# Performance work log

Hardware: AMD Instinct MI355X
Metric: run time of the kernel (lower is better)

## Reference

```python
import jax, jax.numpy as jnp
import numpy as np

N_NODES = 8192
ADJ_LEN = 4096  # first half of codebook = adjective nodes, rest = noun nodes
E_DIM = 256
TOPK = 4
BETA = 0.25


def setup_inputs() -> dict:
    key = jax.random.key(0)
    ks = jax.random.split(key, 6)
    z = jax.random.normal(ks[0], (64, 2 * E_DIM, 16, 16), dtype=jnp.float32)
    node_x = jax.random.normal(ks[1], (N_NODES, 1024), dtype=jnp.float32)
    edge_index = jax.random.randint(ks[2], (2, 131072), 0, N_NODES, dtype=jnp.int32)
    W1 = jax.random.normal(ks[3], (1024, E_DIM), dtype=jnp.float32) * 0.02
    b1 = jnp.zeros((E_DIM,), dtype=jnp.float32)
    W2 = jax.random.normal(ks[4], (E_DIM, E_DIM), dtype=jnp.float32) * 0.02
    b2 = jnp.zeros((E_DIM,), dtype=jnp.float32)
    return {"z": z, "node_x": node_x, "edge_index": edge_index,
            "W1": W1, "b1": b1, "W2": W2, "b2": b2}


def gcn_conv(x, edge_index, W, b):
    # GCNConv: symmetric-normalized adjacency with self-loops, then linear.
    n = x.shape[0]
    loop = jnp.arange(n, dtype=edge_index.dtype)
    src = jnp.concatenate([edge_index[0], loop])
    dst = jnp.concatenate([edge_index[1], loop])
    xw = x @ W  # [n, out]
    deg = jax.ops.segment_sum(jnp.ones_like(dst, dtype=xw.dtype), dst, num_segments=n)
    dinv = jax.lax.rsqrt(jnp.maximum(deg, 1e-12))
    norm = dinv[src] * dinv[dst]  # [E+n]
    out = jax.ops.segment_sum(norm[:, None] * xw[src], dst, num_segments=n)
    return out + b


def pairwise_sqdist(zf, emb):
    # ||z||^2 + ||e||^2 - 2 z.e  -> [M, K]
    return (jnp.sum(zf * zf, axis=1, keepdims=True)
            + jnp.sum(emb * emb, axis=1)
            - 2.0 * zf @ emb.T)


def reference(z, node_x, edge_index, W1, b1, W2, b2):
    sg = jax.lax.stop_gradient
    # GCN over codebook graph (eval mode: dropout is identity)
    h = jax.nn.relu(gcn_conv(node_x, edge_index, W1, b1))
    tew = gcn_conv(h, edge_index, W2, b2)  # [N_NODES, E_DIM]

    b, c2, H, W = z.shape
    # ---- adjective branch: top-k gather + mean ----
    z_adj = jnp.transpose(z[:, :E_DIM], (0, 2, 3, 1))  # b h w c
    zf = z_adj.reshape(-1, E_DIM)  # [M, e_dim]
    emb_a = tew[:ADJ_LEN]
    d = pairwise_sqdist(zf, emb_a)
    _, idx1 = jax.lax.top_k(-d, TOPK)  # [M, topk] smallest distances
    z_adj_q = emb_a[idx1].mean(axis=1).reshape(z_adj.shape)

    quan_loss = jnp.mean((sg(z_adj_q) - z_adj) ** 2)
    commit_loss = BETA * jnp.mean((z_adj_q - sg(z_adj)) ** 2)
    loss = quan_loss + commit_loss
    z_adj_q = z_adj + sg(z_adj_q - z_adj)  # straight-through
    z_adj_q = jnp.transpose(z_adj_q, (0, 3, 1, 2))
    ind1 = idx1.reshape(b, H * W * TOPK)  # sane_index_shape, c=256

    # ---- noun branch: argmin ----
    z_noun = jnp.transpose(z[:, E_DIM:], (0, 2, 3, 1))
    zf = z_noun.reshape(-1, E_DIM)
    emb_n = tew[ADJ_LEN:]
    d = pairwise_sqdist(zf, emb_n)
    idx2 = jnp.argmin(d, axis=1)  # [M]
    z_noun_q = emb_n[idx2].reshape(z_noun.shape)

    q2 = jnp.mean((sg(z_noun_q) - z_noun) ** 2)
    c2_ = BETA * jnp.mean((z_noun_q - sg(z_noun)) ** 2)
    loss = loss + q2 + c2_
    commit_loss = commit_loss + c2_
    quan_loss = quan_loss + q2
    z_noun_q = z_noun + sg(z_noun_q - z_noun)
    z_noun_q = jnp.transpose(z_noun_q, (0, 3, 1, 2))
    ind2 = idx2.reshape(b, H * W)

    z_q = jnp.concatenate([z_adj_q, z_noun_q], axis=1)
    indices = jnp.concatenate([ind1, ind2], axis=1)
    return z_q, loss, commit_loss, quan_loss, indices
```

## Files before the change

kernel.cpp:

```cpp
#include <hip/hip_runtime.h>

#define N_NODES 8192
#define N_EDGES 131072
#define E_DIM 256
#define NE_HALF 4096
#define LOSS_OFF 8388608
#define IDX_OFF 8388611
#define KC_PANEL 384

#define WS_DINV 0
#define WS_EN2 8192
#define WS_LOSS 16384
#define WS_CNT 17408
#define WS_ROWSTART 25600
#define WS_FILL 34816
#define WS_COL 43008
#define WS_XW 174080
#define WS_H  2271232
#define WS_TEW 4368384
#define WS_QN2 6465536

__global__ void count_kernel(const int* __restrict__ dst, int* __restrict__ cnt) {
    int e = blockIdx.x * blockDim.x + threadIdx.x;
    if (e < N_EDGES) atomicAdd(&cnt[dst[e]], 1);
}

__global__ __launch_bounds__(1024) void scan_kernel(const int* __restrict__ cnt,
                                                    int* __restrict__ rowstart,
                                                    float* __restrict__ dinv) {
    __shared__ int part[1024];
    int t = threadIdx.x;
    int c[8], pre[8];
    int run = 0;
#pragma unroll
    for (int i = 0; i < 8; ++i) {
        c[i] = cnt[t * 8 + i];
        pre[i] = run;
        run += c[i];
    }
    part[t] = run;
    __syncthreads();
    for (int d = 1; d < 1024; d <<= 1) {
        int add = (t >= d) ? part[t - d] : 0;
        __syncthreads();
        part[t] += add;
        __syncthreads();
    }
    int off = (t == 0) ? 0 : part[t - 1];
#pragma unroll
    for (int i = 0; i < 8; ++i) {
        rowstart[t * 8 + i] = off + pre[i];
        dinv[t * 8 + i] = 1.0f / sqrtf((float)(c[i] + 1));
    }
    if (t == 1023) rowstart[8192] = part[1023];
}

__global__ void scatter_kernel(const int* __restrict__ dst,
                               const int* __restrict__ rowstart, int* __restrict__ fill,
                               int* __restrict__ col) {
    int e = blockIdx.x * blockDim.x + threadIdx.x;
    if (e < N_EDGES) {
        int d = dst[e];
        int pos = atomicAdd(&fill[d], 1);
        col[rowstart[d] + pos] = e;
    }
}

__global__ __launch_bounds__(256) void sort_kernel(const int* __restrict__ src,
                                                   const int* __restrict__ rowstart,
                                                   int* __restrict__ col) {
    int i = blockIdx.x * blockDim.x + threadIdx.x;
    if (i >= N_NODES) return;
    int s0 = rowstart[i], s1 = rowstart[i + 1];
    for (int a = s0 + 1; a < s1; ++a) {
        int v = col[a];
        int b = a - 1;
        while (b >= s0 && col[b] > v) { col[b + 1] = col[b]; --b; }
        col[b + 1] = v;
    }
    for (int a = s0; a < s1; ++a) col[a] = src[col[a]];
}

__global__ __launch_bounds__(256) void gemm_kernel(const float* __restrict__ X,
                                                   const float* __restrict__ W,
                                                   float* __restrict__ Y, int K) {
    __shared__ float aT[16][68];
    __shared__ float bT[16][68];
    const int t = threadIdx.x;
    const int bm = blockIdx.x * 64;
    const int bn = blockIdx.y * 64;
    float cacc[4][4] = {};
    const int tm = t >> 4, tn = t & 15;
    const int lm = t >> 2, lk = (t & 3) * 4;
    const int bk = t >> 4, bn4 = (t & 15) * 4;
    int kp = 0;
    bool first = true;
    while (kp < K) {
        int rem = K - kp;
        int pl;
        if (rem >= 2 * KC_PANEL) pl = KC_PANEL;
        else if (rem > KC_PANEL) pl = (rem / 2 + 15) & ~15;
        else pl = rem;
        const int kend = kp + pl;
        float pacc[4][4] = {};
        for (int k0 = kp; k0 < kend; k0 += 16) {
            __syncthreads();
            float4 av = *(const float4*)&X[(size_t)(bm + lm) * K + k0 + lk];
            aT[lk + 0][lm] = av.x; aT[lk + 1][lm] = av.y;
            aT[lk + 2][lm] = av.z; aT[lk + 3][lm] = av.w;
            *(float4*)&bT[bk][bn4] = *(const float4*)&W[(size_t)(k0 + bk) * E_DIM + bn + bn4];
            __syncthreads();
#pragma unroll
            for (int k = 0; k < 16; ++k) {
                float4 a = *(const float4*)&aT[k][tm * 4];
                float4 b = *(const float4*)&bT[k][tn * 4];
                float qa[4] = {a.x, a.y, a.z, a.w};
                float ea[4] = {b.x, b.y, b.z, b.w};
#pragma unroll
                for (int i = 0; i < 4; ++i)
#pragma unroll
                    for (int j = 0; j < 4; ++j) pacc[i][j] = fmaf(qa[i], ea[j], pacc[i][j]);
            }
        }
        if (first) {
#pragma unroll
            for (int i = 0; i < 4; ++i)
#pragma unroll
                for (int j = 0; j < 4; ++j) cacc[i][j] = pacc[i][j];
        } else {
#pragma unroll
            for (int i = 0; i < 4; ++i)
#pragma unroll
                for (int j = 0; j < 4; ++j) cacc[i][j] = __fadd_rn(cacc[i][j], pacc[i][j]);
        }
        first = false;
        kp = kend;
    }
#pragma unroll
    for (int i = 0; i < 4; ++i) {
        float4 v = make_float4(cacc[i][0], cacc[i][1], cacc[i][2], cacc[i][3]);
        *(float4*)&Y[(size_t)(bm + tm * 4 + i) * E_DIM + bn + tn * 4] = v;
    }
}

__global__ __launch_bounds__(256) void agg_kernel(const float* __restrict__ xw,
                                                  const int* __restrict__ rowstart,
                                                  const int* __restrict__ col,
                                                  const float* __restrict__ dinv,
                                                  const float* __restrict__ bias,
                                                  float* __restrict__ out, int do_relu) {
    int i = blockIdx.x;
    int c = threadIdx.x;
    float di = dinv[i];
    float acc = 0.0f;
    int s0 = rowstart[i], s1 = rowstart[i + 1];
    for (int j = s0; j < s1; ++j) {
        int s = col[j];
        float nrm = __fmul_rn(dinv[s], di);
        acc = __fadd_rn(acc, __fmul_rn(nrm, xw[(size_t)s * E_DIM + c]));
    }
    acc = __fadd_rn(acc, __fmul_rn(__fmul_rn(di, di), xw[(size_t)i * E_DIM + c]));
    acc = __fadd_rn(acc, bias[c]);
    if (do_relu) acc = fmaxf(acc, 0.0f);
    out[(size_t)i * E_DIM + c] = acc;
}

__global__ __launch_bounds__(256) void enorm_kernel(const float* __restrict__ e,
                                                    float* __restrict__ out) {
    int t = threadIdx.x;
    int row = blockIdx.x * 16 + (t >> 4);
    int l = t & 15;
    int blk = l >> 3, j = l & 7;
    const float* p = e + (size_t)row * 256 + blk * 128 + j;
    float v = p[0];
    float acc = __fmul_rn(v, v);
#pragma unroll
    for (int i = 1; i < 16; ++i) {
        float w = p[i * 8];
        acc = __fadd_rn(acc, __fmul_rn(w, w));
    }
    acc = __fadd_rn(acc, __shfl_xor(acc, 1, 64));
    acc = __fadd_rn(acc, __shfl_xor(acc, 2, 64));
    acc = __fadd_rn(acc, __shfl_xor(acc, 4, 64));
    acc = __fadd_rn(acc, __shfl_xor(acc, 8, 64));
    if (l == 0) out[row] = acc;
}

__global__ __launch_bounds__(256) void qnorm_kernel(const float* __restrict__ z,
                                                    float* __restrict__ out) {
    int t = threadIdx.x;
    int row = blockIdx.x * 16 + (t >> 4);
    int half = row >> 14, r = row & 16383;
    int b = r >> 8, pp = r & 255;
    int l = t & 15;
    int blk = l >> 3, j = l & 7;
    const float* p = z + (size_t)b * 131072 + (size_t)half * 65536 + pp +
                     (size_t)(blk * 128 + j) * 256;
    float v = p[0];
    float acc = __fmul_rn(v, v);
#pragma unroll
    for (int i = 1; i < 16; ++i) {
        float w = p[(size_t)i * 8 * 256];
        acc = __fadd_rn(acc, __fmul_rn(w, w));
    }
    acc = __fadd_rn(acc, __shfl_xor(acc, 1, 64));
    acc = __fadd_rn(acc, __shfl_xor(acc, 2, 64));
    acc = __fadd_rn(acc, __shfl_xor(acc, 4, 64));
    acc = __fadd_rn(acc, __shfl_xor(acc, 8, 64));
    if (l == 0) out[row] = acc;
}

template <int TK>
__global__ __launch_bounds__(256) void quant_kernel(const float* __restrict__ z,
                                                    const float* __restrict__ emb,
                                                    const float* __restrict__ en2,
                                                    const float* __restrict__ qn2,
                                                    float* __restrict__ out,
                                                    float* __restrict__ lossAcc, int coff) {
    __shared__ float qT[E_DIM][36];
    __shared__ float eT[32][132];
    __shared__ float sEn2[128];
    __shared__ int sIdx[32][TK];
    __shared__ float red[256];

    const int t = threadIdx.x;
    const int r0 = blockIdx.x * 32;
    const int b = r0 >> 8;
    const int p0 = r0 & 255;

    {
        const int q = t & 31;
        const int kk = t >> 5;
        const float* zb = z + (size_t)b * 131072 + (size_t)coff * 256 + (p0 + q);
#pragma unroll
        for (int i = 0; i < 32; ++i) {
            int k = kk + 8 * i;
            qT[k][q] = zb[(size_t)k * 256];
        }
    }

    const int tq = t >> 5;
    const int te = t & 31;
    const int q0 = tq * 4;
    const int e0 = te * 4;
    const int sk = (t & 7) * 4;
    const int se = t >> 3;

    float aq[4];
#pragma unroll
    for (int i = 0; i < 4; ++i) aq[i] = qn2[r0 + q0 + i];

    float bsr[4][TK];
    int bir[4][TK];
#pragma unroll
    for (int i = 0; i < 4; ++i)
#pragma unroll
        for (int j = 0; j < TK; ++j) { bsr[i][j] = 3.4e38f; bir[i][j] = 0; }

    for (int et = 0; et < NE_HALF / 128; ++et) {
        const int ebase = et * 128;
        float acc[4][4] = {};
        for (int kc = 0; kc < 8; ++kc) {
            __syncthreads();
#pragma unroll
            for (int i = 0; i < 4; ++i) {
                int e = se + 32 * i;
                float4 v = *(const float4*)&emb[(size_t)(ebase + e) * E_DIM + kc * 32 + sk];
                eT[sk + 0][e] = v.x; eT[sk + 1][e] = v.y;
                eT[sk + 2][e] = v.z; eT[sk + 3][e] = v.w;
            }
            if (kc == 0 && t < 128) sEn2[t] = en2[ebase + t];
            __syncthreads();
#pragma unroll 8
            for (int k = 0; k < 32; ++k) {
                float4 qv = *(const float4*)&qT[kc * 32 + k][q0];
                float4 ev = *(const float4*)&eT[k][e0];
                float qa[4] = {qv.x, qv.y, qv.z, qv.w};
                float ea[4] = {ev.x, ev.y, ev.z, ev.w};
#pragma unroll
                for (int i = 0; i < 4; ++i)
#pragma unroll
                    for (int j = 0; j < 4; ++j) acc[i][j] = fmaf(qa[i], ea[j], acc[i][j]);
            }
        }
#pragma unroll
        for (int j = 0; j < 4; ++j) {
            float e2 = sEn2[e0 + j];
            int gi = ebase + e0 + j;
#pragma unroll
            for (int i = 0; i < 4; ++i) {
                float t1 = __fadd_rn(aq[i], e2);
                float s = __fsub_rn(t1, __fmul_rn(2.0f, acc[i][j]));
                if (s < bsr[i][TK - 1]) {
                    bsr[i][TK - 1] = s; bir[i][TK - 1] = gi;
#pragma unroll
                    for (int m = TK - 1; m > 0; --m) {
                        if (bsr[i][m] < bsr[i][m - 1]) {
                            float tf = bsr[i][m]; bsr[i][m] = bsr[i][m - 1]; bsr[i][m - 1] = tf;
                            int ti2 = bir[i][m]; bir[i][m] = bir[i][m - 1]; bir[i][m - 1] = ti2;
                        }
                    }
                }
            }
        }
    }

#pragma unroll
    for (int m = 1; m < 32; m <<= 1) {
#pragma unroll
        for (int i = 0; i < 4; ++i) {
            float ms[TK], os[TK], ns[TK];
            int mi[TK], oi[TK], ni[TK];
#pragma unroll
            for (int j = 0; j < TK; ++j) {
                ms[j] = bsr[i][j]; mi[j] = bir[i][j];
                os[j] = __shfl_xor(bsr[i][j], m, 64);
                oi[j] = __shfl_xor(bir[i][j], m, 64);
            }
#pragma unroll
            for (int x = 0; x < TK; ++x) {
                bool ta = (ms[0] < os[0]) || (ms[0] == os[0] && mi[0] < oi[0]);
                ns[x] = ta ? ms[0] : os[0];
                ni[x] = ta ? mi[0] : oi[0];
#pragma unroll
                for (int y = 0; y < TK - 1; ++y) {
                    ms[y] = ta ? ms[y + 1] : ms[y];
                    mi[y] = ta ? mi[y + 1] : mi[y];
                    os[y] = ta ? os[y] : os[y + 1];
                    oi[y] = ta ? oi[y] : oi[y + 1];
                }
            }
#pragma unroll
            for (int j = 0; j < TK; ++j) { bsr[i][j] = ns[j]; bir[i][j] = ni[j]; }
        }
    }

    if (te == 0) {
#pragma unroll
        for (int i = 0; i < 4; ++i) {
            int q = q0 + i;
            int r = r0 + q, bb = r >> 8, pp = r & 255;
#pragma unroll
            for (int j = 0; j < TK; ++j) sIdx[q][j] = bir[i][j];
            if (TK == 4) {
#pragma unroll
                for (int j = 0; j < TK; ++j)
                    out[IDX_OFF + (size_t)bb * 1280 + pp * 4 + j] = (float)bir[i][j];
            } else {
                out[IDX_OFF + (size_t)bb * 1280 + 1024 + pp] = (float)bir[i][0];
            }
        }
    }
    __syncthreads();

    float lsum = 0.0f;
    {
        const int q = t & 31;
        const int r = r0 + q, bb = r >> 8, pp = r & 255;
        float* ob = out + (size_t)bb * 131072 + (size_t)coff * 256 + pp;
        int id[TK];
#pragma unroll
        for (int j = 0; j < TK; ++j) id[j] = sIdx[q][j];
        const float inv = 1.0f / (float)TK;
        for (int i = 0; i < 32; ++i) {
            int c = (t >> 5) + 8 * i;
            float v = 0.0f;
#pragma unroll
            for (int j = 0; j < TK; ++j) v = __fadd_rn(v, emb[(size_t)id[j] * E_DIM + c]);
            v *= inv;
            float dd = v - qT[c][q];
            lsum += dd * dd;
            ob[(size_t)c * 256] = v;
        }
    }
    red[t] = lsum;
    __syncthreads();
    for (int s2 = 128; s2 > 0; s2 >>= 1) {
        if (t < s2) red[t] += red[t + s2];
        __syncthreads();
    }
    if (t == 0) atomicAdd(lossAcc, red[0]);
}

__global__ void final_kernel(const float* __restrict__ lossAcc, float* __restrict__ out) {
    if (threadIdx.x == 0 && blockIdx.x == 0) {
        const float inv = 1.0f / 4194304.0f;
        float mseA = lossAcc[0] * inv;
        float mseN = lossAcc[1] * inv;
        float quan = mseA + mseN;
        float commit = 0.25f * mseA + 0.25f * mseN;
        out[LOSS_OFF + 0] = quan + commit;
        out[LOSS_OFF + 1] = commit;
        out[LOSS_OFF + 2] = quan;
    }
}

extern "C" void kernel_launch(void* const* d_in, const int* in_sizes, int n_in,
                              void* d_out, int out_size, void* d_ws, size_t ws_size,
                              hipStream_t stream) {
    const float* z = (const float*)d_in[0];
    const float* node_x = (const float*)d_in[1];
    const int* ei = (const int*)d_in[2];
    const float* W1 = (const float*)d_in[3];
    const float* b1 = (const float*)d_in[4];
    const float* W2 = (const float*)d_in[5];
    const float* b2 = (const float*)d_in[6];
    float* out = (float*)d_out;
    float* ws = (float*)d_ws;

    float* dinv = ws + WS_DINV;
    float* en2 = ws + WS_EN2;
    float* lossAcc = ws + WS_LOSS;
    int* cnt = (int*)(ws + WS_CNT);
    int* rowstart = (int*)(ws + WS_ROWSTART);
    int* fill = (int*)(ws + WS_FILL);
    int* col = (int*)(ws + WS_COL);
    float* xw = ws + WS_XW;
    float* h = ws + WS_H;
    float* tew = ws + WS_TEW;
    float* qn2 = ws + WS_QN2;

    const int* srcp = ei;
    const int* dstp = ei + N_EDGES;

    hipMemsetAsync(cnt, 0, N_NODES * sizeof(int), stream);
    hipMemsetAsync(fill, 0, N_NODES * sizeof(int), stream);
    hipMemsetAsync(lossAcc, 0, 2 * sizeof(float), stream);

    count_kernel<<<N_EDGES / 256, 256, 0, stream>>>(dstp, cnt);
    scan_kernel<<<1, 1024, 0, stream>>>(cnt, rowstart, dinv);
    scatter_kernel<<<N_EDGES / 256, 256, 0, stream>>>(dstp, rowstart, fill, col);
    sort_kernel<<<N_NODES / 256, 256, 0, stream>>>(srcp, rowstart, col);

    qnorm_kernel<<<2048, 256, 0, stream>>>(z, qn2);

    gemm_kernel<<<dim3(128, 4), 256, 0, stream>>>(node_x, W1, xw, 1024);
    agg_kernel<<<N_NODES, 256, 0, stream>>>(xw, rowstart, col, dinv, b1, h, 1);
    gemm_kernel<<<dim3(128, 4), 256, 0, stream>>>(h, W2, xw, 256);
    agg_kernel<<<N_NODES, 256, 0, stream>>>(xw, rowstart, col, dinv, b2, tew, 0);

    enorm_kernel<<<512, 256, 0, stream>>>(tew, en2);

    quant_kernel<4><<<512, 256, 0, stream>>>(z, tew, en2, qn2, out, lossAcc + 0, 0);
    quant_kernel<1><<<512, 256, 0, stream>>>(z, tew + (size_t)NE_HALF * E_DIM,
                                             en2 + NE_HALF, qn2 + 16384, out,
                                             lossAcc + 1, 256);
    final_kernel<<<1, 64, 0, stream>>>(lossAcc, out);
}
```

Measured before the change: 1.585 ms.

## Split codebook search across blocks with packed-key top-k and separate merge kernels

The distance/top-k search is split along the codebook dimension, so each block handles a slice of embeddings with a larger register tile (4 or 8 queries by 8 embeddings per thread), and partial top-k lists go to workspace. New merge kernels combine the partial lists, write indices, gather the quantized vectors and accumulate the losses. Distance and index are packed into one 64-bit key, which turns the comparisons and shuffles into single-word operations, and the shared-memory embedding tile uses an XOR swizzle to avoid bank conflicts. The cost is extra launches and a workspace round trip, plus higher register pressure from the bigger tiles. The packed key relies on the float bits ordering correctly as unsigned integers, which holds only for non-negative distances.

New measurement: 1.820 ms. 14.8% more time.

```diff
diff --git a/kernel.cpp b/kernel.cpp
--- a/kernel.cpp
+++ b/kernel.cpp
@@ -210,165 +210,276 @@
     if (l == 0) out[row] = acc;
 }
 
-template <int TK>
-__global__ __launch_bounds__(256) void quant_kernel(const float* __restrict__ z,
-                                                    const float* __restrict__ emb,
-                                                    const float* __restrict__ en2,
-                                                    const float* __restrict__ qn2,
-                                                    float* __restrict__ out,
-                                                    float* __restrict__ lossAcc, int coff) {
-    __shared__ float qT[E_DIM][36];
-    __shared__ float eT[32][132];
-    __shared__ float sEn2[128];
-    __shared__ int sIdx[32][TK];
+__device__ __forceinline__ unsigned long long shfl_xor_u64(unsigned long long v, int m) {
+    unsigned int lo = (unsigned int)v, hi = (unsigned int)(v >> 32);
+    lo = __shfl_xor(lo, m, 64);
+    hi = __shfl_xor(hi, m, 64);
+    return ((unsigned long long)hi << 32) | lo;
+}
+
+template <int TK, int QM>
+__device__ __forceinline__ void quant_body(const float* __restrict__ z,
+                                           const float* __restrict__ emb,
+                                           const float* __restrict__ en2,
+                                           const float* __restrict__ qn2,
+                                           unsigned long long* __restrict__ topWs,
+                                           int coff) {
+    constexpr int EP = QM / 2;
+    constexpr int QB = 8 * QM;
+    constexpr int EPB = NE_HALF / EP;
+    constexpr int NET = EPB / 256;
+    constexpr int QPAD = QB + 8;
+
+    __shared__ float eT[32][264];
+    __shared__ float qS[32][QPAD];
+    __shared__ float sEn2[256];
+
+    const int t = threadIdx.x;
+    const int qt = blockIdx.x / EP;
+    const int ep = blockIdx.x % EP;
+    const int r0 = qt * QB;
+    const int b = r0 >> 8;
+    const int p0 = r0 & 255;
+    const int e00 = ep * EPB;
+
+    const int tq = t >> 5, te = t & 31;
+    const int q0 = tq * QM;
+    const int e0 = te * 4;
+
+    const int sk = (t & 7) * 4;
+    const int se = t >> 3;
+    const int cb = se ^ (sk & 24);
+    const int kq = t >> 3, jq = (t & 7) * 4;
+
+    const float* zb = z + (size_t)b * 131072 + (size_t)coff * 256 + p0;
+
+    float aq[QM];
+#pragma unroll
+    for (int i = 0; i < QM; ++i) aq[i] = qn2[r0 + q0 + i];
+
+    unsigned long long bk[QM][TK];
+#pragma unroll
+    for (int i = 0; i < QM; ++i)
+#pragma unroll
+        for (int j = 0; j < TK; ++j) bk[i][j] = 0xFFFFFFFFFFFFFFFFull;
+
+    for (int et = 0; et < NET; ++et) {
+        const int ebase = e00 + et * 256;
+        float acc[QM][8] = {};
+        for (int kc = 0; kc < 8; ++kc) {
+            __syncthreads();
+#pragma unroll
+            for (int i = 0; i < 8; ++i) {
+                float4 v = *(const float4*)&emb[(size_t)(ebase + se + 32 * i) * 256 + kc * 32 + sk];
+                eT[sk + 0][cb + 32 * i] = v.x;
+                eT[sk + 1][cb + 32 * i] = v.y;
+                eT[sk + 2][cb + 32 * i] = v.z;
+                eT[sk + 3][cb + 32 * i] = v.w;
+            }
+            {
+                float4 v = *(const float4*)&zb[(size_t)(kc * 32 + kq) * 256 + jq];
+                *(float4*)&qS[kq][jq] = v;
+                if (QM == 8) {
+                    float4 w = *(const float4*)&zb[(size_t)(kc * 32 + kq) * 256 + jq + 32];
+                    *(float4*)&qS[kq][jq + 32] = w;
+                }
+            }
+            if (kc == 0) sEn2[t] = en2[ebase + t];
+            __syncthreads();
+#pragma unroll
+            for (int k = 0; k < 32; ++k) {
+                const int f = k & 24;
+                const int c1 = e0 ^ f;
+                float4 ea = *(const float4*)&eT[k][c1];
+                float4 eb = *(const float4*)&eT[k][128 + c1];
+                float ev[8] = {ea.x, ea.y, ea.z, ea.w, eb.x, eb.y, eb.z, eb.w};
+                float qv[QM];
+                {
+                    float4 qa = *(const float4*)&qS[k][q0];
+                    qv[0] = qa.x; qv[1] = qa.y; qv[2] = qa.z; qv[3] = qa.w;
+                    if (QM == 8) {
+                        float4 qb2 = *(const float4*)&qS[k][q0 + 4];
+                        qv[4] = qb2.x; qv[5] = qb2.y; qv[6] = qb2.z; qv[7] = qb2.w;
+                    }
+                }
+#pragma unroll
+                for (int i = 0; i < QM; ++i)
+#pragma unroll
+                    for (int j = 0; j < 8; ++j)
+                        acc[i][j] = fmaf(qv[i], ev[j], acc[i][j]);
+            }
+        }
+#pragma unroll
+        for (int j = 0; j < 8; ++j) {
+            const int le = (j < 4) ? (e0 + j) : (128 + e0 + j - 4);
+            float e2 = sEn2[le];
+            unsigned int gi = (unsigned int)(ebase + le);
+#pragma unroll
+            for (int i = 0; i < QM; ++i) {
+                float t1 = __fadd_rn(aq[i], e2);
+                float s = __fsub_rn(t1, __fmul_rn(2.0f, acc[i][j]));
+                unsigned long long key =
+                    ((unsigned long long)__float_as_uint(s) << 32) | gi;
+                if (key < bk[i][TK - 1]) {
+                    bk[i][TK - 1] = key;
+#pragma unroll
+                    for (int mm = TK - 1; mm > 0; --mm)
+                        if (bk[i][mm] < bk[i][mm - 1]) {
+                            unsigned long long tmp = bk[i][mm];
+                            bk[i][mm] = bk[i][mm - 1];
+                            bk[i][mm - 1] = tmp;
+                        }
+                }
+            }
+        }
+    }
+
+#pragma unroll
+    for (int mw = 1; mw < 32; mw <<= 1) {
+#pragma unroll
+        for (int i = 0; i < QM; ++i) {
+            unsigned long long ms[TK], os[TK], ns[TK];
+#pragma unroll
+            for (int j = 0; j < TK; ++j) {
+                ms[j] = bk[i][j];
+                os[j] = shfl_xor_u64(bk[i][j], mw);
+            }
+#pragma unroll
+            for (int x = 0; x < TK; ++x) {
+                bool ta = ms[0] < os[0];
+                ns[x] = ta ? ms[0] : os[0];
+#pragma unroll
+                for (int y = 0; y < TK - 1; ++y) {
+                    ms[y] = ta ? ms[y + 1] : ms[y];
+                    os[y] = ta ? os[y] : os[y + 1];
+                }
+            }
+#pragma unroll
+            for (int j = 0; j < TK; ++j) bk[i][j] = ns[j];
+        }
+    }
+
+    if (te == 0) {
+#pragma unroll
+        for (int i = 0; i < QM; ++i) {
+            unsigned long long* dst = topWs + ((size_t)(r0 + q0 + i) * EP + ep) * TK;
+#pragma unroll
+            for (int j = 0; j < TK; ++j) dst[j] = bk[i][j];
+        }
+    }
+}
+
+__global__ __launch_bounds__(256, 4) void quantA_kernel(const float* __restrict__ z,
+                                                        const float* __restrict__ emb,
+                                                        const float* __restrict__ en2,
+                                                        const float* __restrict__ qn2,
+                                                        unsigned long long* __restrict__ topWs) {
+    quant_body<4, 4>(z, emb, en2, qn2, topWs, 0);
+}
+
+__global__ __launch_bounds__(256, 3) void quantN_kernel(const float* __restrict__ z,
+                                                        const float* __restrict__ emb,
+                                                        const float* __restrict__ en2,
+                                                        const float* __restrict__ qn2,
+                                                        unsigned long long* __restrict__ topWs) {
+    quant_body<1, 8>(z, emb, en2, qn2, topWs, 256);
+}
+
+__global__ __launch_bounds__(256) void mergeA_kernel(const unsigned long long* __restrict__ topWs,
+                                                     const float* __restrict__ z,
+                                                     const float* __restrict__ emb,
+                                                     float* __restrict__ out,
+                                                     float* __restrict__ lossAcc) {
+    __shared__ int sIdx[32][4];
     __shared__ float red[256];
-
     const int t = threadIdx.x;
     const int r0 = blockIdx.x * 32;
-    const int b = r0 >> 8;
-    const int p0 = r0 & 255;
-
-    {
-        const int q = t & 31;
-        const int kk = t >> 5;
-        const float* zb = z + (size_t)b * 131072 + (size_t)coff * 256 + (p0 + q);
-#pragma unroll
-        for (int i = 0; i < 32; ++i) {
-            int k = kk + 8 * i;
-            qT[k][q] = zb[(size_t)k * 256];
-        }
-    }
-
-    const int tq = t >> 5;
-    const int te = t & 31;
-    const int q0 = tq * 4;
-    const int e0 = te * 4;
-    const int sk = (t & 7) * 4;
-    const int se = t >> 3;
-
-    float aq[4];
-#pragma unroll
-    for (int i = 0; i < 4; ++i) aq[i] = qn2[r0 + q0 + i];
-
-    float bsr[4][TK];
-    int bir[4][TK];
-#pragma unroll
-    for (int i = 0; i < 4; ++i)
-#pragma unroll
-        for (int j = 0; j < TK; ++j) { bsr[i][j] = 3.4e38f; bir[i][j] = 0; }
-
-    for (int et = 0; et < NE_HALF / 128; ++et) {
-        const int ebase = et * 128;
-        float acc[4][4] = {};
-        for (int kc = 0; kc < 8; ++kc) {
-            __syncthreads();
-#pragma unroll
-            for (int i = 0; i < 4; ++i) {
-                int e = se + 32 * i;
-                float4 v = *(const float4*)&emb[(size_t)(ebase + e) * E_DIM + kc * 32 + sk];
-                eT[sk + 0][e] = v.x; eT[sk + 1][e] = v.y;
-                eT[sk + 2][e] = v.z; eT[sk + 3][e] = v.w;
-            }
-            if (kc == 0 && t < 128) sEn2[t] = en2[ebase + t];
-            __syncthreads();
-#pragma unroll 8
-            for (int k = 0; k < 32; ++k) {
-                float4 qv = *(const float4*)&qT[kc * 32 + k][q0];
-                float4 ev = *(const float4*)&eT[k][e0];
-                float qa[4] = {qv.x, qv.y, qv.z, qv.w};
-                float ea[4] = {ev.x, ev.y, ev.z, ev.w};
-#pragma unroll
-                for (int i = 0; i < 4; ++i)
-#pragma unroll
-                    for (int j = 0; j < 4; ++j) acc[i][j] = fmaf(qa[i], ea[j], acc[i][j]);
-            }
-        }
+    const int b = r0 >> 8, p0 = r0 & 255;
+    if (t < 32) {
+        const unsigned long long* src = topWs + (size_t)(r0 + t) * 8;
+        unsigned long long ms[4], os[4], ns[4];
+#pragma unroll
+        for (int j = 0; j < 4; ++j) { ms[j] = src[j]; os[j] = src[4 + j]; }
+#pragma unroll
+        for (int x = 0; x < 4; ++x) {
+            bool ta = ms[0] < os[0];
+            ns[x] = ta ? ms[0] : os[0];
+#pragma unroll
+            for (int y = 0; y < 3; ++y) {
+                ms[y] = ta ? ms[y + 1] : ms[y];
+                os[y] = ta ? os[y] : os[y + 1];
+            }
+        }
+        int pp = p0 + t;
 #pragma unroll
         for (int j = 0; j < 4; ++j) {
-            float e2 = sEn2[e0 + j];
-            int gi = ebase + e0 + j;
-#pragma unroll
-            for (int i = 0; i < 4; ++i) {
-                float t1 = __fadd_rn(aq[i], e2);
-                float s = __fsub_rn(t1, __fmul_rn(2.0f, acc[i][j]));
-                if (s < bsr[i][TK - 1]) {
-                    bsr[i][TK - 1] = s; bir[i][TK - 1] = gi;
-#pragma unroll
-                    for (int m = TK - 1; m > 0; --m) {
-                        if (bsr[i][m] < bsr[i][m - 1]) {
-                            float tf = bsr[i][m]; bsr[i][m] = bsr[i][m - 1]; bsr[i][m - 1] = tf;
-                            int ti2 = bir[i][m]; bir[i][m] = bir[i][m - 1]; bir[i][m - 1] = ti2;
-                        }
-                    }
-                }
-            }
-        }
-    }
-
-#pragma unroll
-    for (int m = 1; m < 32; m <<= 1) {
-#pragma unroll
-        for (int i = 0; i < 4; ++i) {
-            float ms[TK], os[TK], ns[TK];
-            int mi[TK], oi[TK], ni[TK];
-#pragma unroll
-            for (int j = 0; j < TK; ++j) {
-                ms[j] = bsr[i][j]; mi[j] = bir[i][j];
-                os[j] = __shfl_xor(bsr[i][j], m, 64);
-                oi[j] = __shfl_xor(bir[i][j], m, 64);
-            }
-#pragma unroll
-            for (int x = 0; x < TK; ++x) {
-                bool ta = (ms[0] < os[0]) || (ms[0] == os[0] && mi[0] < oi[0]);
-                ns[x] = ta ? ms[0] : os[0];
-                ni[x] = ta ? mi[0] : oi[0];
-#pragma unroll
-                for (int y = 0; y < TK - 1; ++y) {
-                    ms[y] = ta ? ms[y + 1] : ms[y];
-                    mi[y] = ta ? mi[y + 1] : mi[y];
-                    os[y] = ta ? os[y] : os[y + 1];
-                    oi[y] = ta ? oi[y] : oi[y + 1];
-                }
-            }
-#pragma unroll
-            for (int j = 0; j < TK; ++j) { bsr[i][j] = ns[j]; bir[i][j] = ni[j]; }
-        }
-    }
-
-    if (te == 0) {
-#pragma unroll
-        for (int i = 0; i < 4; ++i) {
-            int q = q0 + i;
-            int r = r0 + q, bb = r >> 8, pp = r & 255;
-#pragma unroll
-            for (int j = 0; j < TK; ++j) sIdx[q][j] = bir[i][j];
-            if (TK == 4) {
-#pragma unroll
-                for (int j = 0; j < TK; ++j)
-                    out[IDX_OFF + (size_t)bb * 1280 + pp * 4 + j] = (float)bir[i][j];
-            } else {
-                out[IDX_OFF + (size_t)bb * 1280 + 1024 + pp] = (float)bir[i][0];
-            }
+            int idx = (int)(unsigned int)(ns[j] & 0xffffffffull);
+            sIdx[t][j] = idx;
+            out[IDX_OFF + (size_t)b * 1280 + pp * 4 + j] = (float)idx;
         }
     }
     __syncthreads();
-
     float lsum = 0.0f;
     {
         const int q = t & 31;
-        const int r = r0 + q, bb = r >> 8, pp = r & 255;
-        float* ob = out + (size_t)bb * 131072 + (size_t)coff * 256 + pp;
-        int id[TK];
-#pragma unroll
-        for (int j = 0; j < TK; ++j) id[j] = sIdx[q][j];
-        const float inv = 1.0f / (float)TK;
+        const int pp = p0 + q;
+        float* ob = out + (size_t)b * 131072 + pp;
+        const float* zb = z + (size_t)b * 131072 + pp;
+        int id[4];
+#pragma unroll
+        for (int j = 0; j < 4; ++j) id[j] = sIdx[q][j];
         for (int i = 0; i < 32; ++i) {
             int c = (t >> 5) + 8 * i;
             float v = 0.0f;
 #pragma unroll
-            for (int j = 0; j < TK; ++j) v = __fadd_rn(v, emb[(size_t)id[j] * E_DIM + c]);
-            v *= inv;
-            float dd = v - qT[c][q];
+            for (int j = 0; j < 4; ++j) v = __fadd_rn(v, emb[(size_t)id[j] * 256 + c]);
+            v *= 0.25f;
+            float dd = v - zb[(size_t)c * 256];
+            lsum += dd * dd;
+            ob[(size_t)c * 256] = v;
+        }
+    }
+    red[t] = lsum;
+    __syncthreads();
+    for (int s2 = 128; s2 > 0; s2 >>= 1) {
+        if (t < s2) red[t] += red[t + s2];
+        __syncthreads();
+    }
+    if (t == 0) atomicAdd(lossAcc, red[0]);
+}
+
+__global__ __launch_bounds__(256) void mergeN_kernel(const unsigned long long* __restrict__ topWs,
+                                                     const float* __restrict__ z,
+                                                     const float* __restrict__ emb,
+                                                     float* __restrict__ out,
+                                                     float* __restrict__ lossAcc) {
+    __shared__ int sIdx[32];
+    __shared__ float red[256];
+    const int t = threadIdx.x;
+    const int r0 = blockIdx.x * 32;
+    const int b = r0 >> 8, p0 = r0 & 255;
+    if (t < 32) {
+        const unsigned long long* src = topWs + (size_t)(r0 + t) * 4;
+        unsigned long long k0 = src[0], k1 = src[1], k2 = src[2], k3 = src[3];
+        unsigned long long m0 = (k0 < k1) ? k0 : k1;
+        unsigned long long m1 = (k2 < k3) ? k2 : k3;
+        unsigned long long mm = (m0 < m1) ? m0 : m1;
+        int idx = (int)(unsigned int)(mm & 0xffffffffull);
+        sIdx[t] = idx;
+        out[IDX_OFF + (size_t)b * 1280 + 1024 + p0 + t] = (float)idx;
+    }
+    __syncthreads();
+    float lsum = 0.0f;
+    {
+        const int q = t & 31;
+        const int pp = p0 + q;
+        float* ob = out + (size_t)b * 131072 + 65536 + pp;
+        const float* zb = z + (size_t)b * 131072 + 65536 + pp;
+        int id = sIdx[q];
+        for (int i = 0; i < 32; ++i) {
+            int c = (t >> 5) + 8 * i;
+            float v = emb[(size_t)id * 256 + c];
+            float dd = v - zb[(size_t)c * 256];
             lsum += dd * dd;
             ob[(size_t)c * 256] = v;
         }
@@ -419,6 +530,8 @@
     float* h = ws + WS_H;
     float* tew = ws + WS_TEW;
     float* qn2 = ws + WS_QN2;
+    unsigned long long* topA = (unsigned long long*)(ws + WS_XW);
+    unsigned long long* topN = topA + 131072;
 
     const int* srcp = ei;
     const int* dstp = ei + N_EDGES;
@@ -441,9 +554,11 @@
 
     enorm_kernel<<<512, 256, 0, stream>>>(tew, en2);
 
-    quant_kernel<4><<<512, 256, 0, stream>>>(z, tew, en2, qn2, out, lossAcc + 0, 0);
-    quant_kernel<1><<<512, 256, 0, stream>>>(z, tew + (size_t)NE_HALF * E_DIM,
-                                             en2 + NE_HALF, qn2 + 16384, out,
-                                             lossAcc + 1, 256);
+    quantA_kernel<<<1024, 256, 0, stream>>>(z, tew, en2, qn2, topA);
+    quantN_kernel<<<1024, 256, 0, stream>>>(z, tew + (size_t)NE_HALF * E_DIM,
+                                            en2 + NE_HALF, qn2 + 16384, topN);
+    mergeA_kernel<<<512, 256, 0, stream>>>(topA, z, tew, out, lossAcc + 0);
+    mergeN_kernel<<<512, 256, 0, stream>>>(topN, z, tew + (size_t)NE_HALF * E_DIM,
+                                           out, lossAcc + 1);
     final_kernel<<<1, 64, 0, stream>>>(lossAcc, out);
 }
```
